# Performance work log

Measured on AMD Instinct MI355X. Metric: run time of the kernel, lower is better.

## Reference

```python
import jax, jax.numpy as jnp
import numpy as np

N_EMBED = 1024
EMBED_DIM = 64
DECAY = 0.99
EPS = 1e-05


def setup_inputs() -> dict:
    key = jax.random.key(0)
    k1, k2 = jax.random.split(key)
    z_e = jax.random.normal(k1, (16, 4096, EMBED_DIM), dtype=jnp.float32)
    # torch init: uniform_(-1/n_embed, 1/n_embed)
    embed = (jax.random.uniform(k2, (N_EMBED, EMBED_DIM), dtype=jnp.float32) * 2.0 - 1.0) / N_EMBED
    cluster_size = jnp.zeros((N_EMBED,), dtype=jnp.float32)
    embed_avg = embed.copy()
    return {"z_e": z_e, "embed": embed, "cluster_size": cluster_size, "embed_avg": embed_avg}


def reference(z_e, embed, cluster_size, embed_avg):
    B, N, E = z_e.shape
    flat = z_e.reshape(-1, E)  # [T, E], T = B*N
    dist = (jnp.sum(flat * flat, axis=1, keepdims=True)
            - 2.0 * flat @ embed.T
            + jnp.sum(embed * embed, axis=1)[None, :])  # [T, K]
    embed_ind = jnp.argmin(dist, axis=1)  # argmax(-dist)
    z_q = embed[embed_ind].reshape(B, N, E)

    # training-mode EMA statistics (scatter-add == one-hot matmul, but memory-efficient)
    onehot_sum = jnp.zeros((N_EMBED,), flat.dtype).at[embed_ind].add(1.0)
    embed_sum = jnp.zeros((N_EMBED, E), flat.dtype).at[embed_ind].add(flat)
    new_cluster_size = DECAY * cluster_size + (1.0 - DECAY) * onehot_sum
    new_embed_avg = DECAY * embed_avg + (1.0 - DECAY) * embed_sum
    n = jnp.sum(new_cluster_size)
    cs = (new_cluster_size + EPS) / (n + N_EMBED * EPS) * n
    new_embed = new_embed_avg / cs[:, None]

    diff = jnp.mean((jax.lax.stop_gradient(z_q) - z_e) ** 2)
    z_q_st = z_e + jax.lax.stop_gradient(z_q - z_e)  # straight-through
    return (z_q_st, diff, embed_ind.reshape(B, N), new_embed, new_cluster_size, new_embed_avg)
```

## Files before the change

### kernel.cpp

```cpp
#include <hip/hip_runtime.h>
#include <math.h>

#define T_TOK 65536
#define K_CODE 1024
#define E_DIM 64
#define DECAYF 0.99f
#define EPSF 1e-5f

#define TT 256
#define QCAP 2048
#define HACC 1.3e-3f

typedef short short8 __attribute__((ext_vector_type(8)));
typedef float f32x16 __attribute__((ext_vector_type(16)));

__device__ __forceinline__ float mul_nf(float a, float b) {
#pragma clang fp contract(off)
    return a * b;
}
__device__ __forceinline__ float add_nf(float a, float b) {
#pragma clang fp contract(off)
    return a + b;
}
__device__ __forceinline__ float sub_nf(float a, float b) {
#pragma clang fp contract(off)
    return a - b;
}

__device__ __forceinline__ float np_sq_row(const float* xrow) {
    const float4* xp = reinterpret_cast<const float4*>(xrow);
    float r[8];
#pragma unroll
    for (int g = 0; g < 8; ++g) {
        float4 va = xp[2 * g], vb = xp[2 * g + 1];
        float e[8] = {va.x, va.y, va.z, va.w, vb.x, vb.y, vb.z, vb.w};
#pragma unroll
        for (int j = 0; j < 8; ++j) {
            if (g == 0) r[j] = mul_nf(e[j], e[j]);
            else        r[j] = add_nf(r[j], mul_nf(e[j], e[j]));
        }
    }
    float s01 = add_nf(r[0], r[1]);
    float s23 = add_nf(r[2], r[3]);
    float s45 = add_nf(r[4], r[5]);
    float s67 = add_nf(r[6], r[7]);
    return add_nf(add_nf(s01, s23), add_nf(s45, s67));
}

__device__ __forceinline__ unsigned f2bf_rne(float f) {
    unsigned u = __float_as_uint(f);
    u += 0x7FFFu + ((u >> 16) & 1u);
    return (u >> 16);
}

__device__ __forceinline__ void exact_key(int t0, int tl, int code,
                                          const float* __restrict__ z_e,
                                          const float* __restrict__ embed,
                                          const float* xn_s, const float* wn_s,
                                          unsigned long long* key_s) {
    const float4* xp = reinterpret_cast<const float4*>(z_e + (size_t)(t0 + tl) * E_DIM);
    const float4* wp = reinterpret_cast<const float4*>(embed + (size_t)code * E_DIM);
    float d = 0.f;
#pragma unroll
    for (int m = 0; m < 16; ++m) {
        float4 x4 = xp[m];
        float4 w4 = wp[m];
        d = __builtin_fmaf(x4.x, w4.x, d);
        d = __builtin_fmaf(x4.y, w4.y, d);
        d = __builtin_fmaf(x4.z, w4.z, d);
        d = __builtin_fmaf(x4.w, w4.w, d);
    }
    float dist = add_nf(sub_nf(xn_s[tl], d + d), wn_s[code]);
    unsigned b = __float_as_uint(dist);
    unsigned mk = (b & 0x80000000u) ? ~b : (b | 0x80000000u);
    atomicMin(key_s + tl, ((unsigned long long)mk << 32) | (unsigned)code);
}


__global__ __launch_bounds__(1024, 4) void dist_kernel(const float* __restrict__ z_e,
                                                       const float* __restrict__ embed,
                                                       float* __restrict__ out_zq,
                                                       float* __restrict__ out_ind,
                                                       float* __restrict__ diff_acc,
                                                       float* __restrict__ esum_rep,
                                                       float* __restrict__ onehot_rep,
                                                       int rep_mask) {
    __shared__ unsigned short Ws[K_CODE * E_DIM];
    __shared__ float wn_s[K_CODE];
    __shared__ float xn_s[TT];
    __shared__ float m_s[2][TT];
    __shared__ unsigned long long key_s[TT];
    __shared__ unsigned q_s[QCAP];
    __shared__ int qc_s;

    int tid = threadIdx.x;
    int lane = tid & 63;
    int wave = tid >> 6;
    int g = lane >> 5;
    int tg = wave & 7;
    int ch = wave >> 3;
    int t0 = blockIdx.x * TT;

    if (tid == 0) qc_s = 0;
    if (tid < TT) {
        key_s[tid] = ~0ull;
        xn_s[tid] = np_sq_row(z_e + (size_t)(t0 + tid) * E_DIM);
    }

    {
        int row = tid;
        const float4* wp = reinterpret_cast<const float4*>(embed + (size_t)row * E_DIM);
        uint4* WsQ = reinterpret_cast<uint4*>(Ws);
        float r8[8];
#pragma unroll
        for (int gq = 0; gq < 8; ++gq) {
            float4 va = wp[2 * gq], vb = wp[2 * gq + 1];
            float e[8] = {va.x, va.y, va.z, va.w, vb.x, vb.y, vb.z, vb.w};
#pragma unroll
            for (int j = 0; j < 8; ++j) {
                if (gq == 0) r8[j] = mul_nf(e[j], e[j]);
                else         r8[j] = add_nf(r8[j], mul_nf(e[j], e[j]));
            }
            unsigned p0 = f2bf_rne(e[0]) | (f2bf_rne(e[1]) << 16);
            unsigned p1 = f2bf_rne(e[2]) | (f2bf_rne(e[3]) << 16);
            unsigned p2 = f2bf_rne(e[4]) | (f2bf_rne(e[5]) << 16);
            unsigned p3 = f2bf_rne(e[6]) | (f2bf_rne(e[7]) << 16);
            WsQ[row * 8 + (gq ^ (row & 7))] = make_uint4(p0, p1, p2, p3);
        }
        float s01 = add_nf(r8[0], r8[1]);
        float s23 = add_nf(r8[2], r8[3]);
        float s45 = add_nf(r8[4], r8[5]);
        float s67 = add_nf(r8[6], r8[7]);
        wn_s[row] = add_nf(add_nf(s01, s23), add_nf(s45, s67));
    }

    int arow = tg * 32 + (lane & 31);
    const float* xrow = z_e + (size_t)(t0 + arow) * E_DIM;
    short8 afr[4];
#pragma unroll
    for (int kc = 0; kc < 4; ++kc) {
        int base = kc * 16 + g * 8;
        float4 a = *reinterpret_cast<const float4*>(xrow + base);
        float4 b = *reinterpret_cast<const float4*>(xrow + base + 4);
        afr[kc][0] = (short)f2bf_rne(a.x);
        afr[kc][1] = (short)f2bf_rne(a.y);
        afr[kc][2] = (short)f2bf_rne(a.z);
        afr[kc][3] = (short)f2bf_rne(a.w);
        afr[kc][4] = (short)f2bf_rne(b.x);
        afr[kc][5] = (short)f2bf_rne(b.y);
        afr[kc][6] = (short)f2bf_rne(b.z);
        afr[kc][7] = (short)f2bf_rne(b.w);
    }

    __syncthreads();

    float maxr[16];
#pragma unroll
    for (int r = 0; r < 16; ++r) maxr[r] = -INFINITY;

#pragma unroll 2
    for (int tt = 0; tt < 16; ++tt) {
        int code = (ch * 16 + tt) * 32 + (lane & 31);
        f32x16 acc;
#pragma unroll
        for (int i = 0; i < 16; ++i) acc[i] = 0.f;
#pragma unroll
        for (int kc = 0; kc < 4; ++kc) {
            int ps = (2 * kc + g) ^ (code & 7);
            short8 bfr = *reinterpret_cast<const short8*>(&Ws[code * E_DIM + ps * 8]);
            acc = __builtin_amdgcn_mfma_f32_32x32x16_bf16(afr[kc], bfr, acc, 0, 0, 0);
        }
#pragma unroll
        for (int r = 0; r < 16; ++r) maxr[r] = fmaxf(maxr[r], acc[r]);
    }

#pragma unroll
    for (int off = 1; off < 32; off <<= 1) {
#pragma unroll
        for (int r = 0; r < 16; ++r)
            maxr[r] = fmaxf(maxr[r], __shfl_xor(maxr[r], off, 64));
    }
    if ((lane & 31) == 0) {
#pragma unroll
        for (int r = 0; r < 16; ++r) {
            int row = (r & 3) + 8 * (r >> 2) + 4 * g;
            m_s[ch][tg * 32 + row] = maxr[r];
        }
    }
    __syncthreads();

    float thr[16];
#pragma unroll
    for (int r = 0; r < 16; ++r) {
        int row = (r & 3) + 8 * (r >> 2) + 4 * g;
        int tok = tg * 32 + row;
        thr[r] = fmaxf(m_s[0][tok], m_s[1][tok]) - HACC;
    }

#pragma unroll 2
    for (int tt = 0; tt < 16; ++tt) {
        int code = (ch * 16 + tt) * 32 + (lane & 31);
        f32x16 acc;
#pragma unroll
        for (int i = 0; i < 16; ++i) acc[i] = 0.f;
#pragma unroll
        for (int kc = 0; kc < 4; ++kc) {
            int ps = (2 * kc + g) ^ (code & 7);
            short8 bfr = *reinterpret_cast<const short8*>(&Ws[code * E_DIM + ps * 8]);
            acc = __builtin_amdgcn_mfma_f32_32x32x16_bf16(afr[kc], bfr, acc, 0, 0, 0);
        }
        float tmax = -INFINITY;
#pragma unroll
        for (int r = 0; r < 16; ++r) tmax = fmaxf(tmax, acc[r] - thr[r]);
        if (tmax >= 0.f) {
#pragma unroll
            for (int r = 0; r < 16; ++r) {
                if (acc[r] >= thr[r]) {
                    int row = (r & 3) + 8 * (r >> 2) + 4 * g;
                    int tl = tg * 32 + row;
                    int slot = atomicAdd(&qc_s, 1);
                    if (slot < QCAP)
                        q_s[slot] = ((unsigned)tl << 10) | (unsigned)code;
                    else
                        exact_key(t0, tl, code, z_e, embed, xn_s, wn_s, key_s);
                }
            }
        }
    }
    __syncthreads();

    int qn = qc_s;
    if (qn > QCAP) qn = QCAP;
    for (int e = tid; e < qn; e += 1024) {
        unsigned q = q_s[e];
        int tl = (int)(q >> 10);
        int code = (int)(q & 1023u);
        exact_key(t0, tl, code, z_e, embed, xn_s, wn_s, key_s);
    }
    __syncthreads();

    if (tid < TT) out_ind[t0 + tid] = (float)(unsigned)(key_s[tid] & 1023ull);

    int rep = blockIdx.x & rep_mask;
    float* esum = esum_rep + (size_t)rep * (K_CODE * E_DIM);
    float* onehot = onehot_rep + (size_t)rep * K_CODE;

    float ds = 0.f;
#pragma unroll 4
    for (int it = 0; it < 16; ++it) {
        int tl = wave * 16 + it;
        int bi = (int)(unsigned)(key_s[tl] & 1023ull);
        float xv = z_e[(size_t)(t0 + tl) * E_DIM + lane];
        float wv = embed[(size_t)bi * E_DIM + lane];
        float rr = sub_nf(wv, xv);
        out_zq[(size_t)(t0 + tl) * E_DIM + lane] = add_nf(xv, rr);
        ds = __builtin_fmaf(rr, rr, ds);
        atomicAdd(&esum[(size_t)bi * E_DIM + lane], xv);
        if (lane == 0) atomicAdd(&onehot[bi], 1.0f);
    }
#pragma unroll
    for (int o = 32; o > 0; o >>= 1) ds += __shfl_down(ds, o, 64);
    if (lane == 0) atomicAdd(diff_acc, ds);
}

__global__ __launch_bounds__(1024) void finalize_cs_kernel(const float* __restrict__ cluster_size,
                                                           const float* __restrict__ onehot_rep,
                                                           const float* __restrict__ ws_diff,
                                                           float* __restrict__ out_diff,
                                                           float* __restrict__ out_ncs,
                                                           float* __restrict__ ws_n,
                                                           int nrep) {
    int k = threadIdx.x;
    float oh = 0.f;
    for (int r = 0; r < nrep; ++r) oh += onehot_rep[(size_t)r * K_CODE + k];
    float ncs = DECAYF * cluster_size[k] + (1.0f - DECAYF) * oh;
    out_ncs[k] = ncs;

    __shared__ float red[1024];
    red[k] = ncs;
    __syncthreads();
#pragma unroll
    for (int s = 512; s > 0; s >>= 1) {
        if (k < s) red[k] += red[k + s];
        __syncthreads();
    }
    if (k == 0) {
        ws_n[0] = red[0];
        out_diff[0] = ws_diff[0] * (1.0f / 4194304.0f);
    }
}

__global__ __launch_bounds__(256) void finalize_embed_kernel(const float* __restrict__ embed_avg,
                                                             const float* __restrict__ esum_rep,
                                                             const float* __restrict__ out_ncs,
                                                             const float* __restrict__ ws_n,
                                                             float* __restrict__ out_ne,
                                                             float* __restrict__ out_nea,
                                                             int nrep) {
    int gid = blockIdx.x * 256 + threadIdx.x;
    int k = gid >> 4;
    int c = gid & 15;
    float n = ws_n[0];
    float ncs = out_ncs[k];
    float cs = (ncs + EPSF) / (n + (float)K_CODE * EPSF) * n;

    size_t off = (size_t)k * E_DIM + (size_t)c * 4;
    float4 s4 = make_float4(0.f, 0.f, 0.f, 0.f);
    for (int r = 0; r < nrep; ++r) {
        float4 v = *reinterpret_cast<const float4*>(esum_rep + (size_t)r * (K_CODE * E_DIM) + off);
        s4.x += v.x; s4.y += v.y; s4.z += v.z; s4.w += v.w;
    }
    float4 a = *reinterpret_cast<const float4*>(embed_avg + off);
    float4 nea, ne;
    nea.x = DECAYF * a.x + (1.0f - DECAYF) * s4.x;
    nea.y = DECAYF * a.y + (1.0f - DECAYF) * s4.y;
    nea.z = DECAYF * a.z + (1.0f - DECAYF) * s4.z;
    nea.w = DECAYF * a.w + (1.0f - DECAYF) * s4.w;
    ne.x = nea.x / cs; ne.y = nea.y / cs; ne.z = nea.z / cs; ne.w = nea.w / cs;
    *reinterpret_cast<float4*>(out_nea + off) = nea;
    *reinterpret_cast<float4*>(out_ne + off) = ne;
}

extern "C" void kernel_launch(void* const* d_in, const int* in_sizes, int n_in,
                              void* d_out, int out_size, void* d_ws, size_t ws_size,
                              hipStream_t stream) {
    const float* z_e = (const float*)d_in[0];
    const float* embed = (const float*)d_in[1];
    const float* cluster_size = (const float*)d_in[2];
    const float* embed_avg = (const float*)d_in[3];

    float* out = (float*)d_out;
    float* o_zq = out;
    float* o_diff = out + 4194304;
    float* o_ind = out + 4194305;
    float* o_ne = out + 4194305 + 65536;
    float* o_ncs = o_ne + 65536;
    float* o_nea = o_ncs + 1024;

    float* ws = (float*)d_ws;
    float* ws_diff = ws + 0;
    float* ws_n = ws + 1;
    float* ws_onehot = ws + 16;
    float* ws_esum = ws + 8208;

    int nrep = 1;
    while (nrep < 8 &&
           (size_t)(8208 + (size_t)(2 * nrep) * 65536) * sizeof(float) <= ws_size)
        nrep *= 2;

    hipMemsetAsync(ws, 0, (size_t)(8208 + (size_t)nrep * 65536) * sizeof(float), stream);

    dist_kernel<<<T_TOK / TT, 1024, 0, stream>>>(z_e, embed, o_zq, o_ind, ws_diff,
                                                 ws_esum, ws_onehot, nrep - 1);
    finalize_cs_kernel<<<1, 1024, 0, stream>>>(cluster_size, ws_onehot, ws_diff,
                                               o_diff, o_ncs, ws_n, nrep);
    finalize_embed_kernel<<<64, 256, 0, stream>>>(embed_avg, ws_esum, o_ncs, ws_n,
                                                  o_ne, o_nea, nrep);
}
```

Measured before the change: 204.2 us.

## Split codebook across two blocks per token tile and merge argmin in a combine kernel

The distance kernel now splits the 1024 codes into two halves handled by separate 512-thread blocks, each writing a packed (distance, index) key per token to workspace. A new combine kernel takes the minimum of the two keys, writes z_q, the indices and the diff sum, and scatters the EMA statistics. The two finalize kernels are merged into one that recomputes the cluster-size total in every block. The aim is to halve LDS per block (bf16 codebook half) so more blocks fit and occupancy rises, at the cost of an extra launch, keys traffic through global memory, and a looser per-half threshold that can queue more candidates for exact rechecking.

```diff
diff --git a/kernel.cpp b/kernel.cpp
--- a/kernel.cpp
+++ b/kernel.cpp
@@ -8,6 +8,7 @@
 #define EPSF 1e-5f
 
 #define TT 256
+#define HCODE 512
 #define QCAP 2048
 #define HACC 1.3e-3f
 
@@ -53,10 +54,10 @@
     return (u >> 16);
 }
 
-__device__ __forceinline__ void exact_key(int t0, int tl, int code,
+__device__ __forceinline__ void exact_key(int t0, int tl, int code, float wn,
                                           const float* __restrict__ z_e,
                                           const float* __restrict__ embed,
-                                          const float* xn_s, const float* wn_s,
+                                          const float* xn_s,
                                           unsigned long long* key_s) {
     const float4* xp = reinterpret_cast<const float4*>(z_e + (size_t)(t0 + tl) * E_DIM);
     const float4* wp = reinterpret_cast<const float4*>(embed + (size_t)code * E_DIM);
@@ -70,25 +71,19 @@
         d = __builtin_fmaf(x4.z, w4.z, d);
         d = __builtin_fmaf(x4.w, w4.w, d);
     }
-    float dist = add_nf(sub_nf(xn_s[tl], d + d), wn_s[code]);
+    float dist = add_nf(sub_nf(xn_s[tl], d + d), wn);
     unsigned b = __float_as_uint(dist);
     unsigned mk = (b & 0x80000000u) ? ~b : (b | 0x80000000u);
     atomicMin(key_s + tl, ((unsigned long long)mk << 32) | (unsigned)code);
 }
 
 
-__global__ __launch_bounds__(1024, 4) void dist_kernel(const float* __restrict__ z_e,
-                                                       const float* __restrict__ embed,
-                                                       float* __restrict__ out_zq,
-                                                       float* __restrict__ out_ind,
-                                                       float* __restrict__ diff_acc,
-                                                       float* __restrict__ esum_rep,
-                                                       float* __restrict__ onehot_rep,
-                                                       int rep_mask) {
-    __shared__ unsigned short Ws[K_CODE * E_DIM];
-    __shared__ float wn_s[K_CODE];
+__global__ __launch_bounds__(512) void dist_kernel(const float* __restrict__ z_e,
+                                                   const float* __restrict__ embed,
+                                                   unsigned long long* __restrict__ keys2) {
+    __shared__ unsigned short Ws[HCODE * E_DIM];
+    __shared__ float wn_s[HCODE];
     __shared__ float xn_s[TT];
-    __shared__ float m_s[2][TT];
     __shared__ unsigned long long key_s[TT];
     __shared__ unsigned q_s[QCAP];
     __shared__ int qc_s;
@@ -97,9 +92,9 @@
     int lane = tid & 63;
     int wave = tid >> 6;
     int g = lane >> 5;
-    int tg = wave & 7;
-    int ch = wave >> 3;
-    int t0 = blockIdx.x * TT;
+    int h = blockIdx.x & 1;
+    int t0 = (blockIdx.x >> 1) * TT;
+    int kbase = h * HCODE;
 
     if (tid == 0) qc_s = 0;
     if (tid < TT) {
@@ -109,7 +104,8 @@
 
     {
         int row = tid;
-        const float4* wp = reinterpret_cast<const float4*>(embed + (size_t)row * E_DIM);
+        const float4* wp =
+            reinterpret_cast<const float4*>(embed + (size_t)(kbase + row) * E_DIM);
         uint4* WsQ = reinterpret_cast<uint4*>(Ws);
         float r8[8];
 #pragma unroll
@@ -134,7 +130,7 @@
         wn_s[row] = add_nf(add_nf(s01, s23), add_nf(s45, s67));
     }
 
-    int arow = tg * 32 + (lane & 31);
+    int arow = wave * 32 + (lane & 31);
     const float* xrow = z_e + (size_t)(t0 + arow) * E_DIM;
     short8 afr[4];
 #pragma unroll
@@ -159,15 +155,15 @@
     for (int r = 0; r < 16; ++r) maxr[r] = -INFINITY;
 
 #pragma unroll 2
-    for (int tt = 0; tt < 16; ++tt) {
-        int code = (ch * 16 + tt) * 32 + (lane & 31);
+    for (int tile = 0; tile < 16; ++tile) {
+        int cloc = tile * 32 + (lane & 31);
         f32x16 acc;
 #pragma unroll
         for (int i = 0; i < 16; ++i) acc[i] = 0.f;
 #pragma unroll
         for (int kc = 0; kc < 4; ++kc) {
-            int ps = (2 * kc + g) ^ (code & 7);
-            short8 bfr = *reinterpret_cast<const short8*>(&Ws[code * E_DIM + ps * 8]);
+            int ps = (2 * kc + g) ^ (cloc & 7);
+            short8 bfr = *reinterpret_cast<const short8*>(&Ws[cloc * E_DIM + ps * 8]);
             acc = __builtin_amdgcn_mfma_f32_32x32x16_bf16(afr[kc], bfr, acc, 0, 0, 0);
         }
 #pragma unroll
@@ -180,49 +176,36 @@
         for (int r = 0; r < 16; ++r)
             maxr[r] = fmaxf(maxr[r], __shfl_xor(maxr[r], off, 64));
     }
-    if ((lane & 31) == 0) {
-#pragma unroll
-        for (int r = 0; r < 16; ++r) {
-            int row = (r & 3) + 8 * (r >> 2) + 4 * g;
-            m_s[ch][tg * 32 + row] = maxr[r];
-        }
-    }
-    __syncthreads();
-
-    float thr[16];
-#pragma unroll
-    for (int r = 0; r < 16; ++r) {
-        int row = (r & 3) + 8 * (r >> 2) + 4 * g;
-        int tok = tg * 32 + row;
-        thr[r] = fmaxf(m_s[0][tok], m_s[1][tok]) - HACC;
-    }
+#pragma unroll
+    for (int r = 0; r < 16; ++r) maxr[r] -= HACC;
 
 #pragma unroll 2
-    for (int tt = 0; tt < 16; ++tt) {
-        int code = (ch * 16 + tt) * 32 + (lane & 31);
+    for (int tile = 0; tile < 16; ++tile) {
+        int cloc = tile * 32 + (lane & 31);
         f32x16 acc;
 #pragma unroll
         for (int i = 0; i < 16; ++i) acc[i] = 0.f;
 #pragma unroll
         for (int kc = 0; kc < 4; ++kc) {
-            int ps = (2 * kc + g) ^ (code & 7);
-            short8 bfr = *reinterpret_cast<const short8*>(&Ws[code * E_DIM + ps * 8]);
+            int ps = (2 * kc + g) ^ (cloc & 7);
+            short8 bfr = *reinterpret_cast<const short8*>(&Ws[cloc * E_DIM + ps * 8]);
             acc = __builtin_amdgcn_mfma_f32_32x32x16_bf16(afr[kc], bfr, acc, 0, 0, 0);
         }
         float tmax = -INFINITY;
 #pragma unroll
-        for (int r = 0; r < 16; ++r) tmax = fmaxf(tmax, acc[r] - thr[r]);
+        for (int r = 0; r < 16; ++r) tmax = fmaxf(tmax, acc[r] - maxr[r]);
         if (tmax >= 0.f) {
 #pragma unroll
             for (int r = 0; r < 16; ++r) {
-                if (acc[r] >= thr[r]) {
+                if (acc[r] >= maxr[r]) {
                     int row = (r & 3) + 8 * (r >> 2) + 4 * g;
-                    int tl = tg * 32 + row;
+                    int tl = wave * 32 + row;
                     int slot = atomicAdd(&qc_s, 1);
                     if (slot < QCAP)
-                        q_s[slot] = ((unsigned)tl << 10) | (unsigned)code;
+                        q_s[slot] = ((unsigned)tl << 9) | (unsigned)cloc;
                     else
-                        exact_key(t0, tl, code, z_e, embed, xn_s, wn_s, key_s);
+                        exact_key(t0, tl, kbase + cloc, wn_s[cloc], z_e, embed,
+                                  xn_s, key_s);
                 }
             }
         }
@@ -231,77 +214,128 @@
 
     int qn = qc_s;
     if (qn > QCAP) qn = QCAP;
-    for (int e = tid; e < qn; e += 1024) {
+    for (int e = tid; e < qn; e += 512) {
         unsigned q = q_s[e];
-        int tl = (int)(q >> 10);
-        int code = (int)(q & 1023u);
-        exact_key(t0, tl, code, z_e, embed, xn_s, wn_s, key_s);
-    }
-    __syncthreads();
-
-    if (tid < TT) out_ind[t0 + tid] = (float)(unsigned)(key_s[tid] & 1023ull);
-
+        int tl = (int)(q >> 9);
+        int cloc = (int)(q & 511u);
+        exact_key(t0, tl, kbase + cloc, wn_s[cloc], z_e, embed, xn_s, key_s);
+    }
+    __syncthreads();
+
+    if (tid < TT) keys2[(size_t)(t0 + tid) * 2 + h] = key_s[tid];
+}
+
+__global__ __launch_bounds__(256) void combine_kernel(const float* __restrict__ z_e,
+                                                      const float* __restrict__ embed,
+                                                      const unsigned long long* __restrict__ keys2,
+                                                      float* __restrict__ out_zq,
+                                                      float* __restrict__ out_ind,
+                                                      float* __restrict__ diff_acc,
+                                                      float* __restrict__ esum_rep,
+                                                      float* __restrict__ onehot_rep,
+                                                      int rep_mask) {
+    __shared__ int sidx[64];
+    __shared__ float sred[4];
+    int tid = threadIdx.x;
+    int t0 = blockIdx.x * 64;
+
+    if (tid < 64) {
+        unsigned long long k0 = keys2[(size_t)(t0 + tid) * 2];
+        unsigned long long k1 = keys2[(size_t)(t0 + tid) * 2 + 1];
+        unsigned long long kv = k0 < k1 ? k0 : k1;
+        int bi = (int)(kv & 0x3FFull);
+        sidx[tid] = bi;
+        out_ind[t0 + tid] = (float)bi;
+    }
+    __syncthreads();
+
+    float ds = 0.f;
+#pragma unroll
+    for (int u = 0; u < 4; ++u) {
+        int v = u * 256 + tid;
+        int tl = v >> 4;
+        int c = v & 15;
+        int bi = sidx[tl];
+        float4 w4 = *reinterpret_cast<const float4*>(embed + (size_t)bi * E_DIM + c * 4);
+        float4 x4 = *reinterpret_cast<const float4*>(z_e + (size_t)(t0 + tl) * E_DIM + c * 4);
+        float rx = sub_nf(w4.x, x4.x);
+        float ry = sub_nf(w4.y, x4.y);
+        float rz = sub_nf(w4.z, x4.z);
+        float rw = sub_nf(w4.w, x4.w);
+        float4 o;
+        o.x = add_nf(x4.x, rx);
+        o.y = add_nf(x4.y, ry);
+        o.z = add_nf(x4.z, rz);
+        o.w = add_nf(x4.w, rw);
+        *reinterpret_cast<float4*>(out_zq + (size_t)(t0 + tl) * E_DIM + c * 4) = o;
+        ds = __builtin_fmaf(rx, rx, ds);
+        ds = __builtin_fmaf(ry, ry, ds);
+        ds = __builtin_fmaf(rz, rz, ds);
+        ds = __builtin_fmaf(rw, rw, ds);
+    }
+#pragma unroll
+    for (int o = 32; o > 0; o >>= 1) ds += __shfl_down(ds, o, 64);
+    if ((tid & 63) == 0) sred[tid >> 6] = ds;
+    __syncthreads();
+    if (tid == 0) atomicAdd(diff_acc, sred[0] + sred[1] + sred[2] + sred[3]);
+
+    int lane = tid & 63;
+    int wv = tid >> 6;
     int rep = blockIdx.x & rep_mask;
     float* esum = esum_rep + (size_t)rep * (K_CODE * E_DIM);
     float* onehot = onehot_rep + (size_t)rep * K_CODE;
-
-    float ds = 0.f;
-#pragma unroll 4
-    for (int it = 0; it < 16; ++it) {
-        int tl = wave * 16 + it;
-        int bi = (int)(unsigned)(key_s[tl] & 1023ull);
+#pragma unroll
+    for (int j = 0; j < 16; ++j) {
+        int tl = wv * 16 + j;
+        int bi = sidx[tl];
         float xv = z_e[(size_t)(t0 + tl) * E_DIM + lane];
-        float wv = embed[(size_t)bi * E_DIM + lane];
-        float rr = sub_nf(wv, xv);
-        out_zq[(size_t)(t0 + tl) * E_DIM + lane] = add_nf(xv, rr);
-        ds = __builtin_fmaf(rr, rr, ds);
         atomicAdd(&esum[(size_t)bi * E_DIM + lane], xv);
         if (lane == 0) atomicAdd(&onehot[bi], 1.0f);
     }
-#pragma unroll
-    for (int o = 32; o > 0; o >>= 1) ds += __shfl_down(ds, o, 64);
-    if (lane == 0) atomicAdd(diff_acc, ds);
-}
-
-__global__ __launch_bounds__(1024) void finalize_cs_kernel(const float* __restrict__ cluster_size,
-                                                           const float* __restrict__ onehot_rep,
-                                                           const float* __restrict__ ws_diff,
-                                                           float* __restrict__ out_diff,
-                                                           float* __restrict__ out_ncs,
-                                                           float* __restrict__ ws_n,
-                                                           int nrep) {
-    int k = threadIdx.x;
-    float oh = 0.f;
-    for (int r = 0; r < nrep; ++r) oh += onehot_rep[(size_t)r * K_CODE + k];
-    float ncs = DECAYF * cluster_size[k] + (1.0f - DECAYF) * oh;
-    out_ncs[k] = ncs;
-
-    __shared__ float red[1024];
-    red[k] = ncs;
-    __syncthreads();
-#pragma unroll
+}
+
+__global__ __launch_bounds__(256) void finalize_kernel(const float* __restrict__ cluster_size,
+                                                       const float* __restrict__ onehot_rep,
+                                                       const float* __restrict__ ws_diff,
+                                                       const float* __restrict__ embed_avg,
+                                                       const float* __restrict__ esum_rep,
+                                                       float* __restrict__ out_diff,
+                                                       float* __restrict__ out_ncs,
+                                                       float* __restrict__ out_ne,
+                                                       float* __restrict__ out_nea,
+                                                       int nrep) {
+    __shared__ float ncs_s[K_CODE];
+    __shared__ float red[K_CODE];
+    int tid = threadIdx.x;
+
+#pragma unroll
+    for (int i = 0; i < 4; ++i) {
+        int k = tid + 256 * i;
+        float oh = 0.f;
+        for (int r = 0; r < nrep; ++r) oh += onehot_rep[(size_t)r * K_CODE + k];
+        float ncs = DECAYF * cluster_size[k] + (1.0f - DECAYF) * oh;
+        ncs_s[k] = ncs;
+        red[k] = ncs;
+    }
+    __syncthreads();
     for (int s = 512; s > 0; s >>= 1) {
-        if (k < s) red[k] += red[k + s];
+        for (int idx = tid; idx < s; idx += 256) red[idx] += red[idx + s];
         __syncthreads();
     }
-    if (k == 0) {
-        ws_n[0] = red[0];
-        out_diff[0] = ws_diff[0] * (1.0f / 4194304.0f);
-    }
-}
-
-__global__ __launch_bounds__(256) void finalize_embed_kernel(const float* __restrict__ embed_avg,
-                                                             const float* __restrict__ esum_rep,
-                                                             const float* __restrict__ out_ncs,
-                                                             const float* __restrict__ ws_n,
-                                                             float* __restrict__ out_ne,
-                                                             float* __restrict__ out_nea,
-                                                             int nrep) {
-    int gid = blockIdx.x * 256 + threadIdx.x;
-    int k = gid >> 4;
-    int c = gid & 15;
-    float n = ws_n[0];
-    float ncs = out_ncs[k];
+    float n = red[0];
+
+    if (blockIdx.x == 0) {
+#pragma unroll
+        for (int i = 0; i < 4; ++i) {
+            int k = tid + 256 * i;
+            out_ncs[k] = ncs_s[k];
+        }
+        if (tid == 0) out_diff[0] = ws_diff[0] * (1.0f / 4194304.0f);
+    }
+
+    int k = blockIdx.x * 16 + (tid >> 4);
+    int c = tid & 15;
+    float ncs = ncs_s[k];
     float cs = (ncs + EPSF) / (n + (float)K_CODE * EPSF) * n;
 
     size_t off = (size_t)k * E_DIM + (size_t)c * 4;
@@ -339,21 +373,22 @@
 
     float* ws = (float*)d_ws;
     float* ws_diff = ws + 0;
-    float* ws_n = ws + 1;
     float* ws_onehot = ws + 16;
-    float* ws_esum = ws + 8208;
 
     int nrep = 1;
     while (nrep < 8 &&
-           (size_t)(8208 + (size_t)(2 * nrep) * 65536) * sizeof(float) <= ws_size)
+           (size_t)(8208 + (size_t)(2 * nrep) * 65536 + 262144) * sizeof(float) <= ws_size)
         nrep *= 2;
 
+    float* ws_esum = ws + 8208;
+    unsigned long long* ws_keys2 =
+        (unsigned long long*)(ws + 8208 + (size_t)nrep * 65536);
+
     hipMemsetAsync(ws, 0, (size_t)(8208 + (size_t)nrep * 65536) * sizeof(float), stream);
 
-    dist_kernel<<<T_TOK / TT, 1024, 0, stream>>>(z_e, embed, o_zq, o_ind, ws_diff,
-                                                 ws_esum, ws_onehot, nrep - 1);
-    finalize_cs_kernel<<<1, 1024, 0, stream>>>(cluster_size, ws_onehot, ws_diff,
-                                               o_diff, o_ncs, ws_n, nrep);
-    finalize_embed_kernel<<<64, 256, 0, stream>>>(embed_avg, ws_esum, o_ncs, ws_n,
-                                                  o_ne, o_nea, nrep);
-}
+    dist_kernel<<<(T_TOK / TT) * 2, 512, 0, stream>>>(z_e, embed, ws_keys2);
+    combine_kernel<<<T_TOK / 64, 256, 0, stream>>>(z_e, embed, ws_keys2, o_zq, o_ind,
+                                                   ws_diff, ws_esum, ws_onehot, nrep - 1);
+    finalize_kernel<<<64, 256, 0, stream>>>(cluster_size, ws_onehot, ws_diff, embed_avg,
+                                            ws_esum, o_diff, o_ncs, o_ne, o_nea, nrep);
+}
```

Measured after the change: 193.7 us. 1.05x faster.

## Fuse finalize kernels and reuse max registers for thresholds in dist kernel

Applied to the files above, without the earlier changes.

Merges the two finalize kernels into one 64-block kernel in which every block recomputes the cluster-size reduction redundantly, removing one launch and the global round-trip for n. In dist_kernel the threshold array reuses the maxr registers, the min-blocks-per-CU hint is dropped from launch_bounds, and best indices are cached in a shared int array. The aim is lower register pressure and less launch overhead, at the cost of redundant reduction work in each finalize block.

```diff
diff --git a/kernel.cpp b/kernel.cpp
--- a/kernel.cpp
+++ b/kernel.cpp
@@ -53,10 +53,10 @@
     return (u >> 16);
 }
 
-__device__ __forceinline__ void exact_key(int t0, int tl, int code,
+__device__ __forceinline__ void exact_key(int t0, int tl, int code, float wn,
                                           const float* __restrict__ z_e,
                                           const float* __restrict__ embed,
-                                          const float* xn_s, const float* wn_s,
+                                          const float* xn_s,
                                           unsigned long long* key_s) {
     const float4* xp = reinterpret_cast<const float4*>(z_e + (size_t)(t0 + tl) * E_DIM);
     const float4* wp = reinterpret_cast<const float4*>(embed + (size_t)code * E_DIM);
@@ -70,27 +70,28 @@
         d = __builtin_fmaf(x4.z, w4.z, d);
         d = __builtin_fmaf(x4.w, w4.w, d);
     }
-    float dist = add_nf(sub_nf(xn_s[tl], d + d), wn_s[code]);
+    float dist = add_nf(sub_nf(xn_s[tl], d + d), wn);
     unsigned b = __float_as_uint(dist);
     unsigned mk = (b & 0x80000000u) ? ~b : (b | 0x80000000u);
     atomicMin(key_s + tl, ((unsigned long long)mk << 32) | (unsigned)code);
 }
 
 
-__global__ __launch_bounds__(1024, 4) void dist_kernel(const float* __restrict__ z_e,
-                                                       const float* __restrict__ embed,
-                                                       float* __restrict__ out_zq,
-                                                       float* __restrict__ out_ind,
-                                                       float* __restrict__ diff_acc,
-                                                       float* __restrict__ esum_rep,
-                                                       float* __restrict__ onehot_rep,
-                                                       int rep_mask) {
+__global__ __launch_bounds__(1024) void dist_kernel(const float* __restrict__ z_e,
+                                                    const float* __restrict__ embed,
+                                                    float* __restrict__ out_zq,
+                                                    float* __restrict__ out_ind,
+                                                    float* __restrict__ diff_acc,
+                                                    float* __restrict__ esum_rep,
+                                                    float* __restrict__ onehot_rep,
+                                                    int rep_mask) {
     __shared__ unsigned short Ws[K_CODE * E_DIM];
     __shared__ float wn_s[K_CODE];
     __shared__ float xn_s[TT];
     __shared__ float m_s[2][TT];
     __shared__ unsigned long long key_s[TT];
     __shared__ unsigned q_s[QCAP];
+    __shared__ int bi_s[TT];
     __shared__ int qc_s;
 
     int tid = threadIdx.x;
@@ -189,12 +190,11 @@
     }
     __syncthreads();
 
-    float thr[16];
 #pragma unroll
     for (int r = 0; r < 16; ++r) {
         int row = (r & 3) + 8 * (r >> 2) + 4 * g;
         int tok = tg * 32 + row;
-        thr[r] = fmaxf(m_s[0][tok], m_s[1][tok]) - HACC;
+        maxr[r] = fmaxf(m_s[0][tok], m_s[1][tok]) - HACC;
     }
 
 #pragma unroll 2
@@ -211,18 +211,18 @@
         }
         float tmax = -INFINITY;
 #pragma unroll
-        for (int r = 0; r < 16; ++r) tmax = fmaxf(tmax, acc[r] - thr[r]);
+        for (int r = 0; r < 16; ++r) tmax = fmaxf(tmax, acc[r] - maxr[r]);
         if (tmax >= 0.f) {
 #pragma unroll
             for (int r = 0; r < 16; ++r) {
-                if (acc[r] >= thr[r]) {
+                if (acc[r] >= maxr[r]) {
                     int row = (r & 3) + 8 * (r >> 2) + 4 * g;
                     int tl = tg * 32 + row;
                     int slot = atomicAdd(&qc_s, 1);
                     if (slot < QCAP)
                         q_s[slot] = ((unsigned)tl << 10) | (unsigned)code;
                     else
-                        exact_key(t0, tl, code, z_e, embed, xn_s, wn_s, key_s);
+                        exact_key(t0, tl, code, wn_s[code], z_e, embed, xn_s, key_s);
                 }
             }
         }
@@ -235,11 +235,16 @@
         unsigned q = q_s[e];
         int tl = (int)(q >> 10);
         int code = (int)(q & 1023u);
-        exact_key(t0, tl, code, z_e, embed, xn_s, wn_s, key_s);
-    }
-    __syncthreads();
-
-    if (tid < TT) out_ind[t0 + tid] = (float)(unsigned)(key_s[tid] & 1023ull);
+        exact_key(t0, tl, code, wn_s[code], z_e, embed, xn_s, key_s);
+    }
+    __syncthreads();
+
+    if (tid < TT) {
+        int bi = (int)(unsigned)(key_s[tid] & 1023ull);
+        bi_s[tid] = bi;
+        out_ind[t0 + tid] = (float)bi;
+    }
+    __syncthreads();
 
     int rep = blockIdx.x & rep_mask;
     float* esum = esum_rep + (size_t)rep * (K_CODE * E_DIM);
@@ -249,7 +254,7 @@
 #pragma unroll 4
     for (int it = 0; it < 16; ++it) {
         int tl = wave * 16 + it;
-        int bi = (int)(unsigned)(key_s[tl] & 1023ull);
+        int bi = bi_s[tl];
         float xv = z_e[(size_t)(t0 + tl) * E_DIM + lane];
         float wv = embed[(size_t)bi * E_DIM + lane];
         float rr = sub_nf(wv, xv);
@@ -263,45 +268,48 @@
     if (lane == 0) atomicAdd(diff_acc, ds);
 }
 
-__global__ __launch_bounds__(1024) void finalize_cs_kernel(const float* __restrict__ cluster_size,
-                                                           const float* __restrict__ onehot_rep,
-                                                           const float* __restrict__ ws_diff,
-                                                           float* __restrict__ out_diff,
-                                                           float* __restrict__ out_ncs,
-                                                           float* __restrict__ ws_n,
-                                                           int nrep) {
-    int k = threadIdx.x;
-    float oh = 0.f;
-    for (int r = 0; r < nrep; ++r) oh += onehot_rep[(size_t)r * K_CODE + k];
-    float ncs = DECAYF * cluster_size[k] + (1.0f - DECAYF) * oh;
-    out_ncs[k] = ncs;
-
-    __shared__ float red[1024];
-    red[k] = ncs;
-    __syncthreads();
-#pragma unroll
+__global__ __launch_bounds__(256) void finalize_kernel(const float* __restrict__ cluster_size,
+                                                       const float* __restrict__ onehot_rep,
+                                                       const float* __restrict__ ws_diff,
+                                                       const float* __restrict__ embed_avg,
+                                                       const float* __restrict__ esum_rep,
+                                                       float* __restrict__ out_diff,
+                                                       float* __restrict__ out_ncs,
+                                                       float* __restrict__ out_ne,
+                                                       float* __restrict__ out_nea,
+                                                       int nrep) {
+    __shared__ float ncs_s[K_CODE];
+    __shared__ float red[K_CODE];
+    int tid = threadIdx.x;
+
+#pragma unroll
+    for (int i = 0; i < 4; ++i) {
+        int k = tid + 256 * i;
+        float oh = 0.f;
+        for (int r = 0; r < nrep; ++r) oh += onehot_rep[(size_t)r * K_CODE + k];
+        float ncs = DECAYF * cluster_size[k] + (1.0f - DECAYF) * oh;
+        ncs_s[k] = ncs;
+        red[k] = ncs;
+    }
+    __syncthreads();
     for (int s = 512; s > 0; s >>= 1) {
-        if (k < s) red[k] += red[k + s];
+        for (int idx = tid; idx < s; idx += 256) red[idx] += red[idx + s];
         __syncthreads();
     }
-    if (k == 0) {
-        ws_n[0] = red[0];
-        out_diff[0] = ws_diff[0] * (1.0f / 4194304.0f);
-    }
-}
-
-__global__ __launch_bounds__(256) void finalize_embed_kernel(const float* __restrict__ embed_avg,
-                                                             const float* __restrict__ esum_rep,
-                                                             const float* __restrict__ out_ncs,
-                                                             const float* __restrict__ ws_n,
-                                                             float* __restrict__ out_ne,
-                                                             float* __restrict__ out_nea,
-                                                             int nrep) {
-    int gid = blockIdx.x * 256 + threadIdx.x;
-    int k = gid >> 4;
-    int c = gid & 15;
-    float n = ws_n[0];
-    float ncs = out_ncs[k];
+    float n = red[0];
+
+    if (blockIdx.x == 0) {
+#pragma unroll
+        for (int i = 0; i < 4; ++i) {
+            int k = tid + 256 * i;
+            out_ncs[k] = ncs_s[k];
+        }
+        if (tid == 0) out_diff[0] = ws_diff[0] * (1.0f / 4194304.0f);
+    }
+
+    int k = blockIdx.x * 16 + (tid >> 4);
+    int c = tid & 15;
+    float ncs = ncs_s[k];
     float cs = (ncs + EPSF) / (n + (float)K_CODE * EPSF) * n;
 
     size_t off = (size_t)k * E_DIM + (size_t)c * 4;
@@ -339,21 +347,19 @@
 
     float* ws = (float*)d_ws;
     float* ws_diff = ws + 0;
-    float* ws_n = ws + 1;
     float* ws_onehot = ws + 16;
-    float* ws_esum = ws + 8208;
 
     int nrep = 1;
     while (nrep < 8 &&
            (size_t)(8208 + (size_t)(2 * nrep) * 65536) * sizeof(float) <= ws_size)
         nrep *= 2;
 
+    float* ws_esum = ws + 8208;
+
     hipMemsetAsync(ws, 0, (size_t)(8208 + (size_t)nrep * 65536) * sizeof(float), stream);
 
     dist_kernel<<<T_TOK / TT, 1024, 0, stream>>>(z_e, embed, o_zq, o_ind, ws_diff,
                                                  ws_esum, ws_onehot, nrep - 1);
-    finalize_cs_kernel<<<1, 1024, 0, stream>>>(cluster_size, ws_onehot, ws_diff,
-                                               o_diff, o_ncs, ws_n, nrep);
-    finalize_embed_kernel<<<64, 256, 0, stream>>>(embed_avg, ws_esum, o_ncs, ws_n,
-                                                  o_ne, o_nea, nrep);
-}
+    finalize_kernel<<<64, 256, 0, stream>>>(cluster_size, ws_onehot, ws_diff, embed_avg,
+                                            ws_esum, o_diff, o_ncs, o_ne, o_nea, nrep);
+}
```

New measurement: 210.2 us. +2.9%, slower.
